# Performance work log

Hardware: AMD Instinct MI355X
Metric: run time of the kernel (lower is better)

Reference implementation:

```python
import jax, jax.numpy as jnp
import numpy as np

B, S, D, H = 1, 4096, 1024, 16
HD = D // H  # head_dim = 64
NEG = -1e9


def _rotate_half(x):
    x1, x2 = jnp.split(x, 2, axis=-1)
    return jnp.concatenate([-x2, x1], axis=-1)


def _apply_rope(x, cos, sin):
    # x: [b, s, h, hd]; cos/sin: [s, hd] -> broadcast over batch and heads
    c = cos[None, :, None, :]
    s = sin[None, :, None, :]
    return x * c + _rotate_half(x) * s


def setup_inputs() -> dict:
    key = jax.random.key(0)
    kx, kq, ko = jax.random.split(key, 3)
    x = jax.random.normal(kx, (B, S, D), dtype=jnp.float32)
    # causal additive mask (finite large-negative for safe grads)
    i = jnp.arange(S)
    attn_mask = jnp.where(i[None, :] > i[:, None], NEG, 0.0).astype(jnp.float32)[None, None]
    # standard RoPE tables
    inv_freq = 1.0 / (10000.0 ** (np.arange(0, HD, 2, dtype=np.float32) / HD))
    ang = np.arange(S, dtype=np.float32)[:, None] * inv_freq[None, :]  # [S, HD/2]
    ang = np.concatenate([ang, ang], axis=-1)  # [S, HD]
    rope_cos = jnp.asarray(np.cos(ang))
    rope_sin = jnp.asarray(np.sin(ang))
    W_qkv = jax.random.normal(kq, (D, 3 * D), dtype=jnp.float32) * (D ** -0.5)
    W_out = jax.random.normal(ko, (D, D), dtype=jnp.float32) * (D ** -0.5)
    return {"x": x, "attn_mask": attn_mask, "rope_cos": rope_cos,
            "rope_sin": rope_sin, "W_qkv": W_qkv, "W_out": W_out}


def reference(x, attn_mask, rope_cos, rope_sin, W_qkv, W_out):
    b, s, d = x.shape
    qkv = x @ W_qkv                              # [b, s, 3d]
    q, k, v = jnp.split(qkv, 3, axis=-1)
    q = q.reshape(b, s, H, HD)
    k = k.reshape(b, s, H, HD)
    v = v.reshape(b, s, H, HD)
    q = _apply_rope(q, rope_cos, rope_sin)
    k = _apply_rope(k, rope_cos, rope_sin)
    att = jnp.einsum('bqhd,bkhd->bhqk', q, k) / jnp.sqrt(jnp.float32(HD))
    att = att + attn_mask                        # additive mask broadcast [b,h,s,s]
    att = jax.nn.softmax(att, axis=-1)
    out = jnp.einsum('bhqk,bkhd->bqhd', att, v).reshape(b, s, d)
    return out @ W_out
```

## Files before the change

kernel.cpp:

```cpp
#include <hip/hip_runtime.h>


typedef __attribute__((ext_vector_type(8)))  __bf16 bf16x8;
typedef __attribute__((ext_vector_type(4)))  float  f32x4;
typedef __attribute__((ext_vector_type(16))) float  f32x16;
typedef __attribute__((ext_vector_type(8)))  unsigned short ushort8;
typedef __attribute__((ext_vector_type(4)))  unsigned int   u32x4;

#define MFMA16(a,b,c) __builtin_amdgcn_mfma_f32_16x16x32_bf16((a),(b),(c),0,0,0)
#define MFMA32(a,b,c) __builtin_amdgcn_mfma_f32_32x32x16_bf16((a),(b),(c),0,0,0)

static __device__ __forceinline__ unsigned short f2bf(float f) {
  unsigned int u = __builtin_bit_cast(unsigned int, f);
  u = (u + 0x7FFFu + ((u >> 16) & 1u)) >> 16;
  return (unsigned short)u;
}
static __device__ __forceinline__ float bf2f(unsigned short u) {
  return __builtin_bit_cast(float, (unsigned int)u << 16);
}
static __device__ __forceinline__ unsigned int cvtpk(float a, float b) {
  unsigned int r;
  asm("v_cvt_pk_bf16_f32 %0, %1, %2" : "=v"(r) : "v"(a), "v"(b));
  return r;
}
static __device__ __forceinline__ void plswap(unsigned int& a, unsigned int& b) {
#if __has_builtin(__builtin_amdgcn_permlane32_swap)
  auto r = __builtin_amdgcn_permlane32_swap(a, b, false, false);
  a = r[0]; b = r[1];
#else
  unsigned int xa = (unsigned int)__shfl_xor((int)a, 32);
  unsigned int xb = (unsigned int)__shfl_xor((int)b, 32);
  int lane = __builtin_amdgcn_mbcnt_hi(~0u, __builtin_amdgcn_mbcnt_lo(~0u, 0));
  bool hi = lane >= 32;
  a = hi ? xb : a;
  b = hi ? b : xa;
#endif
}
static __device__ __forceinline__ void gll16(const unsigned short* gp, const unsigned short* lp) {
  unsigned int m0v = __builtin_amdgcn_readfirstlane((unsigned int)(unsigned long long)(uintptr_t)lp);
  asm volatile("s_mov_b32 m0, %0\n\tglobal_load_lds_dwordx4 %1, off"
               :: "s"(m0v), "v"(gp) : "memory");
}
static __device__ __forceinline__ void wait_dma() {
  asm volatile("s_waitcnt vmcnt(0)" ::: "memory");
}

__global__ void convert_x(const float* __restrict__ x, unsigned short* __restrict__ o) {
  int i = (blockIdx.x * 256 + threadIdx.x) * 4;
  float4 v = *reinterpret_cast<const float4*>(x + i);
  ushort4 u;
  u.x = f2bf(v.x); u.y = f2bf(v.y); u.z = f2bf(v.z); u.w = f2bf(v.w);
  *reinterpret_cast<ushort4*>(o + i) = u;
}

__global__ void transpose_w(const float* __restrict__ W, unsigned short* __restrict__ WT,
                            int R, int C) {
  __shared__ float t[32][33];
  int c0 = blockIdx.x * 32, r0 = blockIdx.y * 32;
  int tx = threadIdx.x, ty = threadIdx.y;
#pragma unroll
  for (int i = 0; i < 32; i += 8)
    t[ty + i][tx] = W[(size_t)(r0 + ty + i) * C + c0 + tx];
  __syncthreads();
#pragma unroll
  for (int i = 0; i < 32; i += 8)
    WT[(size_t)(c0 + ty + i) * R + r0 + tx] = f2bf(t[tx][ty + i]);
}

template <typename OutT>
__global__ __launch_bounds__(256) void gemm_lds(const unsigned short* __restrict__ A,
                                                const unsigned short* __restrict__ BT,
                                                OutT* __restrict__ C, int M, int N, int K) {
  __shared__ __align__(16) unsigned short As[128 * 32];
  __shared__ __align__(16) unsigned short Bs[128 * 32];
  int tid = threadIdx.x;
  int lane = tid & 63, w = tid >> 6;
  int wr = w >> 1, wc = w & 1;
  int row0 = blockIdx.y * 128, col0 = blockIdx.x * 128;
  int lr = lane & 15, lk = lane >> 4;
  f32x4 acc[4][4] = {};
  for (int k0 = 0; k0 < K; k0 += 32) {
#pragma unroll
    for (int i = 0; i < 2; ++i) {
      int c = i * 256 + tid;
      int r = c >> 2, cc = (c & 3) * 8;
      gll16(A  + (size_t)(row0 + r) * K + k0 + cc, &As[i * 2048 + w * 512]);
      gll16(BT + (size_t)(col0 + r) * K + k0 + cc, &Bs[i * 2048 + w * 512]);
    }
    wait_dma();
    __syncthreads();
    bf16x8 a[4], b[4];
#pragma unroll
    for (int m = 0; m < 4; m++)
      a[m] = *reinterpret_cast<const bf16x8*>(&As[(wr * 64 + m * 16 + lr) * 32 + lk * 8]);
#pragma unroll
    for (int n = 0; n < 4; n++)
      b[n] = *reinterpret_cast<const bf16x8*>(&Bs[(wc * 64 + n * 16 + lr) * 32 + lk * 8]);
#pragma unroll
    for (int m = 0; m < 4; m++)
#pragma unroll
      for (int n = 0; n < 4; n++)
        acc[m][n] = MFMA16(a[m], b[n], acc[m][n]);
    __syncthreads();
  }
#pragma unroll
  for (int m = 0; m < 4; m++)
#pragma unroll
    for (int n = 0; n < 4; n++)
#pragma unroll
      for (int r = 0; r < 4; r++) {
        size_t off = (size_t)(row0 + wr * 64 + m * 16 + lk * 4 + r) * N + col0 + wc * 64 + n * 16 + lr;
        if constexpr (sizeof(OutT) == 2) C[off] = f2bf(acc[m][n][r]);
        else                             C[off] = acc[m][n][r];
      }
}

__global__ void rope_qk(const unsigned short* __restrict__ qkv,
                        const float* __restrict__ cosb, const float* __restrict__ sinb,
                        unsigned short* __restrict__ Q, unsigned short* __restrict__ K) {
  const float QSCALE = 0.125f * 1.4426950408889634f;
  int idx = blockIdx.x * 256 + threadIdx.x;
  int c = idx & 7, s = (idx >> 3) & 4095, h = idx >> 15;
  int d0 = c * 8;
  int base = s * 3072 + h * 64;
  ushort8 qv  = *reinterpret_cast<const ushort8*>(qkv + base + d0);
  ushort8 qv2 = *reinterpret_cast<const ushort8*>(qkv + base + (d0 ^ 32));
  ushort8 kv  = *reinterpret_cast<const ushort8*>(qkv + base + 1024 + d0);
  ushort8 kv2 = *reinterpret_cast<const ushort8*>(qkv + base + 1024 + (d0 ^ 32));
  float sign = (d0 < 32) ? -1.f : 1.f;
  const float4* cp = reinterpret_cast<const float4*>(cosb + s * 64 + d0);
  const float4* sp = reinterpret_cast<const float4*>(sinb + s * 64 + d0);
  float4 c0 = cp[0], c1 = cp[1], s0 = sp[0], s1 = sp[1];
  float co[8] = {c0.x, c0.y, c0.z, c0.w, c1.x, c1.y, c1.z, c1.w};
  float si[8] = {s0.x, s0.y, s0.z, s0.w, s1.x, s1.y, s1.z, s1.w};
  ushort8 qo, ko;
#pragma unroll
  for (int j = 0; j < 8; ++j) {
    float q = bf2f(qv[j]), q2 = bf2f(qv2[j]);
    float k = bf2f(kv[j]), k2 = bf2f(kv2[j]);
    qo[j] = f2bf((q * co[j] + sign * q2 * si[j]) * QSCALE);
    ko[j] = f2bf(k * co[j] + sign * k2 * si[j]);
  }
  *reinterpret_cast<ushort8*>(Q + (size_t)h * 262144 + (size_t)s * 64 + d0) = qo;
  int tt = s >> 5, ql = s & 31, lo = (d0 >> 3) & 1, f = d0 >> 4;
  size_t koff = (size_t)h * 262144 + (size_t)tt * 2048 + (size_t)f * 512
              + (size_t)(lo * 32 + ql) * 8;
  *reinterpret_cast<ushort8*>(K + koff) = ko;
}

__global__ __launch_bounds__(256) void v_frag_prep(const unsigned short* __restrict__ qkv,
                                                   unsigned short* __restrict__ VF) {
  __shared__ unsigned short tile[32][68];
  int t = blockIdx.x, h = blockIdx.y;
  int tid = threadIdx.x;
  {
    int r = tid >> 3, c8 = (tid & 7) * 8;
    *reinterpret_cast<ushort8*>(&tile[r][c8]) =
        *reinterpret_cast<const ushort8*>(qkv + (size_t)(t * 32 + r) * 3072 + 2048 + h * 64 + c8);
  }
  __syncthreads();
  int f = tid >> 6, lane = tid & 63;
  int ql = lane & 31, lo = lane >> 5;
  int sb = (f & 1) * 16 + lo * 8;
  int d  = (f >> 1) * 32 + ql;
  ushort8 v;
#pragma unroll
  for (int j = 0; j < 8; ++j) v[j] = tile[sb + j][d];
  *reinterpret_cast<ushort8*>(VF + (size_t)h * 262144 + (size_t)t * 2048
                              + (size_t)f * 512 + (size_t)lane * 8) = v;
}

__global__ __launch_bounds__(256) void flash_attn32(const unsigned short* __restrict__ Q,
                                                    const unsigned short* __restrict__ Kf,
                                                    const unsigned short* __restrict__ Vf,
                                                    unsigned short* __restrict__ O) {
  const int S = 4096;
  __shared__ float mrg[3][64][34];
  int flat = blockIdx.x;
  int virt = (flat & 7) * 128 + (flat >> 3);
  int h  = virt >> 6;
  int pr = virt & 63;
  int tid = threadIdx.x;
  int lane = tid & 63, w = tid >> 6;
  int ql = lane & 31, lo = lane >> 5;
  const unsigned short* Qh = Q  + (size_t)h * S * 64;
  const unsigned short* Kh = Kf + (size_t)h * S * 64 + lane * 8;
  const unsigned short* Vh = Vf + (size_t)h * S * 64 + lane * 8;

  auto run_tile = [&](int qt) {
    int q0 = qt * 32;
    const int nt = qt + 1;
    bf16x8 qf[4];
#pragma unroll
    for (int f = 0; f < 4; ++f)
      qf[f] = *reinterpret_cast<const bf16x8*>(Qh + (q0 + ql) * 64 + f * 16 + lo * 8);
    f32x16 oT0 = {}, oT1 = {};
    float l = 0.f;

    for (int t = w; t < nt; t += 4) {
      bf16x8 k0 = *reinterpret_cast<const bf16x8*>(Kh + (size_t)t * 2048);
      bf16x8 k1 = *reinterpret_cast<const bf16x8*>(Kh + (size_t)t * 2048 + 512);
      bf16x8 k2 = *reinterpret_cast<const bf16x8*>(Kh + (size_t)t * 2048 + 1024);
      bf16x8 k3 = *reinterpret_cast<const bf16x8*>(Kh + (size_t)t * 2048 + 1536);
      f32x16 p = {};
      __builtin_amdgcn_s_setprio(1);
      p = MFMA32(k0, qf[0], p);
      p = MFMA32(k1, qf[1], p);
      p = MFMA32(k2, qf[2], p);
      p = MFMA32(k3, qf[3], p);
      __builtin_amdgcn_s_setprio(0);
      const unsigned short* vp = Vh + (size_t)t * 2048;
      bf16x8 v00 = *reinterpret_cast<const bf16x8*>(vp);
      bf16x8 v01 = *reinterpret_cast<const bf16x8*>(vp + 512);
      bf16x8 v10 = *reinterpret_cast<const bf16x8*>(vp + 1024);
      bf16x8 v11 = *reinterpret_cast<const bf16x8*>(vp + 1536);
      if (t == nt - 1) {
#pragma unroll
        for (int r = 0; r < 16; ++r) {
          int kvr = (r & 3) + 8 * (r >> 2) + 4 * lo;
          if (kvr > ql) p[r] = -1e9f;
        }
      }
#pragma unroll
      for (int r = 0; r < 16; ++r) p[r] = __builtin_amdgcn_exp2f(p[r]);
      {
        float s0 = (p[0] + p[1])   + (p[2] + p[3]);
        float s1 = (p[4] + p[5])   + (p[6] + p[7]);
        float s2 = (p[8] + p[9])   + (p[10] + p[11]);
        float s3 = (p[12] + p[13]) + (p[14] + p[15]);
        l += (s0 + s1) + (s2 + s3);
      }
      unsigned int A0 = cvtpk(p[0],  p[1]),  A1 = cvtpk(p[2],  p[3]);
      unsigned int B0 = cvtpk(p[4],  p[5]),  B1 = cvtpk(p[6],  p[7]);
      plswap(A0, B0); plswap(A1, B1);
      u32x4 w0 = {A0, A1, B0, B1};
      bf16x8 P0 = __builtin_bit_cast(bf16x8, w0);
      unsigned int C0 = cvtpk(p[8],  p[9]),  C1 = cvtpk(p[10], p[11]);
      unsigned int D0 = cvtpk(p[12], p[13]), D1 = cvtpk(p[14], p[15]);
      plswap(C0, D0); plswap(C1, D1);
      u32x4 w1 = {C0, C1, D0, D1};
      bf16x8 P1 = __builtin_bit_cast(bf16x8, w1);
      __builtin_amdgcn_s_setprio(1);
      oT0 = MFMA32(v00, P0, oT0);
      oT1 = MFMA32(v10, P0, oT1);
      oT0 = MFMA32(v01, P1, oT0);
      oT1 = MFMA32(v11, P1, oT1);
      __builtin_amdgcn_s_setprio(0);
    }

    if (w > 0) {
#pragma unroll
      for (int r = 0; r < 16; ++r) {
        mrg[w - 1][lane][r]      = oT0[r];
        mrg[w - 1][lane][16 + r] = oT1[r];
      }
      mrg[w - 1][lane][32] = l;
    }
    __syncthreads();
    if (w == 0) {
#pragma unroll
      for (int j = 0; j < 3; ++j) {
#pragma unroll
        for (int r = 0; r < 16; ++r) {
          oT0[r] += mrg[j][lane][r];
          oT1[r] += mrg[j][lane][16 + r];
        }
        l += mrg[j][lane][32];
      }
      l += __shfl_xor(l, 32);
      float rl = 1.0f / l;
      size_t obase = (size_t)(q0 + ql) * 1024 + h * 64;
#pragma unroll
      for (int r = 0; r < 16; ++r) {
        int d = (r & 3) + 8 * (r >> 2) + 4 * lo;
        O[obase + d]      = f2bf(oT0[r] * rl);
        O[obase + 32 + d] = f2bf(oT1[r] * rl);
      }
    }
    __syncthreads();
  };

  run_tile(127 - pr);
  run_tile(pr);
}

extern "C" void kernel_launch(void* const* d_in, const int* in_sizes, int n_in,
                              void* d_out, int out_size, void* d_ws, size_t ws_size,
                              hipStream_t stream) {
  const float* x        = (const float*)d_in[0];
  const float* rope_cos = (const float*)d_in[2];
  const float* rope_sin = (const float*)d_in[3];
  const float* W_qkv    = (const float*)d_in[4];
  const float* W_out    = (const float*)d_in[5];
  float* out = (float*)d_out;

  char* ws = (char*)d_ws;
  const size_t MB = 1u << 20;
  unsigned short* xbf   = (unsigned short*)(ws + 0 * MB);
  unsigned short* WqkvT = (unsigned short*)(ws + 8 * MB);
  unsigned short* WoutT = (unsigned short*)(ws + 14 * MB);
  unsigned short* qkv   = (unsigned short*)(ws + 16 * MB);
  unsigned short* Qb    = (unsigned short*)(ws + 40 * MB);
  unsigned short* Kfb   = (unsigned short*)(ws + 48 * MB);
  unsigned short* Vfb   = (unsigned short*)(ws + 56 * MB);
  unsigned short* Ob    = (unsigned short*)(ws + 64 * MB);

  convert_x<<<4096, 256, 0, stream>>>(x, xbf);
  transpose_w<<<dim3(3072 / 32, 1024 / 32), dim3(32, 8), 0, stream>>>(W_qkv, WqkvT, 1024, 3072);
  transpose_w<<<dim3(1024 / 32, 1024 / 32), dim3(32, 8), 0, stream>>>(W_out, WoutT, 1024, 1024);

  gemm_lds<unsigned short><<<dim3(3072 / 128, 4096 / 128), 256, 0, stream>>>(
      xbf, WqkvT, qkv, 4096, 3072, 1024);

  rope_qk<<<2048, 256, 0, stream>>>(qkv, rope_cos, rope_sin, Qb, Kfb);
  v_frag_prep<<<dim3(128, 16), 256, 0, stream>>>(qkv, Vfb);

  flash_attn32<<<1024, 256, 0, stream>>>(Qb, Kfb, Vfb, Ob);

  gemm_lds<float><<<dim3(1024 / 128, 4096 / 128), 256, 0, stream>>>(
      Ob, WoutT, out, 4096, 1024, 1024);
}
```

Measured before the change: 153.1 us.

## Share LDS-staged K/V tiles across two query tiles with double-buffered DMA

The attention kernel now has each block process two adjacent 32-row query tiles together. Waves split as two per query tile, and each pair splits KV tiles by parity. K and V fragments are copied into double-buffered shared memory with async global-to-LDS loads, so each KV tile is fetched once per block and reused by both query tiles, with the next window prefetched while the current one is computed. This halves the grid to 512 blocks. It adds a block-wide barrier per KV window and reduces the number of parallel blocks in exchange for less global/L2 traffic.

```diff
diff --git a/kernel.cpp b/kernel.cpp
--- a/kernel.cpp
+++ b/kernel.cpp
@@ -175,21 +175,35 @@
                                                     const unsigned short* __restrict__ Vf,
                                                     unsigned short* __restrict__ O) {
   const int S = 4096;
-  __shared__ float mrg[3][64][34];
+  __shared__ __align__(16) unsigned short sbuf[2][4][2048];
+  __shared__ float mrg[2][64][34];
   int flat = blockIdx.x;
-  int virt = (flat & 7) * 128 + (flat >> 3);
-  int h  = virt >> 6;
-  int pr = virt & 63;
+  int virt = (flat & 7) * 64 + (flat >> 3);
+  int h = virt >> 5;
+  int i = virt & 31;
   int tid = threadIdx.x;
   int lane = tid & 63, w = tid >> 6;
+  int qm = w & 1, pp = w >> 1;
   int ql = lane & 31, lo = lane >> 5;
-  const unsigned short* Qh = Q  + (size_t)h * S * 64;
-  const unsigned short* Kh = Kf + (size_t)h * S * 64 + lane * 8;
-  const unsigned short* Vh = Vf + (size_t)h * S * 64 + lane * 8;
-
-  auto run_tile = [&](int qt) {
+  const unsigned short* Qh  = Q  + (size_t)h * S * 64;
+  const unsigned short* KfH = Kf + (size_t)h * S * 64;
+  const unsigned short* VfH = Vf + (size_t)h * S * 64;
+
+  const unsigned short* img_src = (w & 1) ? VfH : KfH;
+  int img_dt = w >> 1;
+  auto stage = [&](int nb, int win) {
+    int t = 2 * win + img_dt;
+    const unsigned short* src = img_src + (size_t)t * 2048;
+    const unsigned short* dst = &sbuf[nb][w][0];
+#pragma unroll
+    for (int j = 0; j < 4; ++j)
+      gll16(src + j * 512 + lane * 8, dst + j * 512);
+  };
+
+  auto run_phase = [&](int base_qt) {
+    int qt = base_qt + qm;
     int q0 = qt * 32;
-    const int nt = qt + 1;
+    int nwin = base_qt / 2 + 1;
     bf16x8 qf[4];
 #pragma unroll
     for (int f = 0; f < 4; ++f)
@@ -197,76 +211,87 @@
     f32x16 oT0 = {}, oT1 = {};
     float l = 0.f;
 
-    for (int t = w; t < nt; t += 4) {
-      bf16x8 k0 = *reinterpret_cast<const bf16x8*>(Kh + (size_t)t * 2048);
-      bf16x8 k1 = *reinterpret_cast<const bf16x8*>(Kh + (size_t)t * 2048 + 512);
-      bf16x8 k2 = *reinterpret_cast<const bf16x8*>(Kh + (size_t)t * 2048 + 1024);
-      bf16x8 k3 = *reinterpret_cast<const bf16x8*>(Kh + (size_t)t * 2048 + 1536);
-      f32x16 p = {};
-      __builtin_amdgcn_s_setprio(1);
-      p = MFMA32(k0, qf[0], p);
-      p = MFMA32(k1, qf[1], p);
-      p = MFMA32(k2, qf[2], p);
-      p = MFMA32(k3, qf[3], p);
-      __builtin_amdgcn_s_setprio(0);
-      const unsigned short* vp = Vh + (size_t)t * 2048;
-      bf16x8 v00 = *reinterpret_cast<const bf16x8*>(vp);
-      bf16x8 v01 = *reinterpret_cast<const bf16x8*>(vp + 512);
-      bf16x8 v10 = *reinterpret_cast<const bf16x8*>(vp + 1024);
-      bf16x8 v11 = *reinterpret_cast<const bf16x8*>(vp + 1536);
-      if (t == nt - 1) {
-#pragma unroll
-        for (int r = 0; r < 16; ++r) {
-          int kvr = (r & 3) + 8 * (r >> 2) + 4 * lo;
-          if (kvr > ql) p[r] = -1e9f;
+    stage(0, 0);
+    wait_dma();
+    __syncthreads();
+    int cb = 0;
+    for (int win = 0; win < nwin; ++win) {
+      if (win + 1 < nwin) stage(cb ^ 1, win + 1);
+      int t = 2 * win + pp;
+      if (t <= qt) {
+        const unsigned short* kb = &sbuf[cb][2 * pp][0];
+        const unsigned short* vb = &sbuf[cb][2 * pp + 1][0];
+        bf16x8 k0 = *reinterpret_cast<const bf16x8*>(kb);
+        bf16x8 k1 = *reinterpret_cast<const bf16x8*>(kb + 512 + lane * 8 - lane * 8);
+        k0 = *reinterpret_cast<const bf16x8*>(kb + 0 * 512 + lane * 8);
+        k1 = *reinterpret_cast<const bf16x8*>(kb + 1 * 512 + lane * 8);
+        bf16x8 k2 = *reinterpret_cast<const bf16x8*>(kb + 2 * 512 + lane * 8);
+        bf16x8 k3 = *reinterpret_cast<const bf16x8*>(kb + 3 * 512 + lane * 8);
+        f32x16 p = {};
+        __builtin_amdgcn_s_setprio(1);
+        p = MFMA32(k0, qf[0], p);
+        p = MFMA32(k1, qf[1], p);
+        p = MFMA32(k2, qf[2], p);
+        p = MFMA32(k3, qf[3], p);
+        __builtin_amdgcn_s_setprio(0);
+        bf16x8 v00 = *reinterpret_cast<const bf16x8*>(vb + 0 * 512 + lane * 8);
+        bf16x8 v01 = *reinterpret_cast<const bf16x8*>(vb + 1 * 512 + lane * 8);
+        bf16x8 v10 = *reinterpret_cast<const bf16x8*>(vb + 2 * 512 + lane * 8);
+        bf16x8 v11 = *reinterpret_cast<const bf16x8*>(vb + 3 * 512 + lane * 8);
+        if (t == qt) {
+#pragma unroll
+          for (int r = 0; r < 16; ++r) {
+            int kvr = (r & 3) + 8 * (r >> 2) + 4 * lo;
+            if (kvr > ql) p[r] = -1e9f;
+          }
         }
-      }
-#pragma unroll
-      for (int r = 0; r < 16; ++r) p[r] = __builtin_amdgcn_exp2f(p[r]);
-      {
-        float s0 = (p[0] + p[1])   + (p[2] + p[3]);
-        float s1 = (p[4] + p[5])   + (p[6] + p[7]);
-        float s2 = (p[8] + p[9])   + (p[10] + p[11]);
-        float s3 = (p[12] + p[13]) + (p[14] + p[15]);
-        l += (s0 + s1) + (s2 + s3);
-      }
-      unsigned int A0 = cvtpk(p[0],  p[1]),  A1 = cvtpk(p[2],  p[3]);
-      unsigned int B0 = cvtpk(p[4],  p[5]),  B1 = cvtpk(p[6],  p[7]);
-      plswap(A0, B0); plswap(A1, B1);
-      u32x4 w0 = {A0, A1, B0, B1};
-      bf16x8 P0 = __builtin_bit_cast(bf16x8, w0);
-      unsigned int C0 = cvtpk(p[8],  p[9]),  C1 = cvtpk(p[10], p[11]);
-      unsigned int D0 = cvtpk(p[12], p[13]), D1 = cvtpk(p[14], p[15]);
-      plswap(C0, D0); plswap(C1, D1);
-      u32x4 w1 = {C0, C1, D0, D1};
-      bf16x8 P1 = __builtin_bit_cast(bf16x8, w1);
-      __builtin_amdgcn_s_setprio(1);
-      oT0 = MFMA32(v00, P0, oT0);
-      oT1 = MFMA32(v10, P0, oT1);
-      oT0 = MFMA32(v01, P1, oT0);
-      oT1 = MFMA32(v11, P1, oT1);
-      __builtin_amdgcn_s_setprio(0);
+#pragma unroll
+        for (int r = 0; r < 16; ++r) p[r] = __builtin_amdgcn_exp2f(p[r]);
+        {
+          float s0 = (p[0] + p[1])   + (p[2] + p[3]);
+          float s1 = (p[4] + p[5])   + (p[6] + p[7]);
+          float s2 = (p[8] + p[9])   + (p[10] + p[11]);
+          float s3 = (p[12] + p[13]) + (p[14] + p[15]);
+          l += (s0 + s1) + (s2 + s3);
+        }
+        unsigned int A0 = cvtpk(p[0],  p[1]),  A1 = cvtpk(p[2],  p[3]);
+        unsigned int B0 = cvtpk(p[4],  p[5]),  B1 = cvtpk(p[6],  p[7]);
+        plswap(A0, B0); plswap(A1, B1);
+        u32x4 w0 = {A0, A1, B0, B1};
+        bf16x8 P0 = __builtin_bit_cast(bf16x8, w0);
+        unsigned int C0 = cvtpk(p[8],  p[9]),  C1 = cvtpk(p[10], p[11]);
+        unsigned int D0 = cvtpk(p[12], p[13]), D1 = cvtpk(p[14], p[15]);
+        plswap(C0, D0); plswap(C1, D1);
+        u32x4 w1 = {C0, C1, D0, D1};
+        bf16x8 P1 = __builtin_bit_cast(bf16x8, w1);
+        __builtin_amdgcn_s_setprio(1);
+        oT0 = MFMA32(v00, P0, oT0);
+        oT1 = MFMA32(v10, P0, oT1);
+        oT0 = MFMA32(v01, P1, oT0);
+        oT1 = MFMA32(v11, P1, oT1);
+        __builtin_amdgcn_s_setprio(0);
+      }
+      wait_dma();
+      __syncthreads();
+      cb ^= 1;
     }
 
-    if (w > 0) {
+    if (pp == 1) {
 #pragma unroll
       for (int r = 0; r < 16; ++r) {
-        mrg[w - 1][lane][r]      = oT0[r];
-        mrg[w - 1][lane][16 + r] = oT1[r];
-      }
-      mrg[w - 1][lane][32] = l;
+        mrg[qm][lane][r]      = oT0[r];
+        mrg[qm][lane][16 + r] = oT1[r];
+      }
+      mrg[qm][lane][32] = l;
     }
     __syncthreads();
-    if (w == 0) {
-#pragma unroll
-      for (int j = 0; j < 3; ++j) {
-#pragma unroll
-        for (int r = 0; r < 16; ++r) {
-          oT0[r] += mrg[j][lane][r];
-          oT1[r] += mrg[j][lane][16 + r];
-        }
-        l += mrg[j][lane][32];
-      }
+    if (pp == 0) {
+#pragma unroll
+      for (int r = 0; r < 16; ++r) {
+        oT0[r] += mrg[qm][lane][r];
+        oT1[r] += mrg[qm][lane][16 + r];
+      }
+      l += mrg[qm][lane][32];
       l += __shfl_xor(l, 32);
       float rl = 1.0f / l;
       size_t obase = (size_t)(q0 + ql) * 1024 + h * 64;
@@ -280,8 +305,8 @@
     __syncthreads();
   };
 
-  run_tile(127 - pr);
-  run_tile(pr);
+  run_phase(126 - 2 * i);
+  run_phase(2 * i);
 }
 
 extern "C" void kernel_launch(void* const* d_in, const int* in_sizes, int n_in,
@@ -315,7 +340,7 @@
   rope_qk<<<2048, 256, 0, stream>>>(qkv, rope_cos, rope_sin, Qb, Kfb);
   v_frag_prep<<<dim3(128, 16), 256, 0, stream>>>(qkv, Vfb);
 
-  flash_attn32<<<1024, 256, 0, stream>>>(Qb, Kfb, Vfb, Ob);
+  flash_attn32<<<512, 256, 0, stream>>>(Qb, Kfb, Vfb, Ob);
 
   gemm_lds<float><<<dim3(1024 / 128, 4096 / 128), 256, 0, stream>>>(
       Ob, WoutT, out, 4096, 1024, 1024);
```

After: 147.9 us. -3.4%, faster.
